# Performance work log

Measured on AMD Instinct MI355X. Metric: run time of the kernel, lower is better.

The kernel has to match this reference:

```python
import jax, jax.numpy as jnp
import numpy as np

B, T, C = 4, 2048, 1024
E, F, K = 8, 2048, 2


def setup_inputs() -> dict:
    key = jax.random.key(0)
    k0, k1, k2, k3 = jax.random.split(key, 4)
    s = lambda d: 1.0 / np.sqrt(d)
    x = jax.random.normal(k0, (B, T, C), dtype=jnp.float32)
    Wr = jax.random.normal(k1, (E, C), dtype=jnp.float32) * s(C)      # router: nn.Linear(C, E) weight [E, C]
    W1 = jax.random.normal(k2, (E, 2 * F, C), dtype=jnp.float32) * s(C)  # per-expert w1 [2F, C]
    W2 = jax.random.normal(k3, (E, C, F), dtype=jnp.float32) * s(F)      # per-expert w2 [C, F]
    return {"x": x, "Wr": Wr, "W1": W1, "W2": W2}


def reference(x, Wr, W1, W2):
    Bb, Tt, Cc = x.shape
    flat = x.reshape(-1, Cc)                         # [N, C]
    N = flat.shape[0]
    # router: top-k then softmax over the k selected logits
    logits = flat @ Wr.T                             # [N, E]
    weights, ids = jax.lax.top_k(logits, K)          # [N, K]
    weights = jax.nn.softmax(weights, axis=-1)
    rows = jnp.arange(N)[:, None]
    router_weights = jnp.zeros((N, E), dtype=flat.dtype).at[rows, ids].add(weights)  # [N, E]
    # all experts on all tokens (dense reference), SwiGLU
    h = jnp.einsum('nc,efc->nef', flat, W1)          # [N, E, 2F]
    val, gate = h[..., :F], h[..., F:]
    act = val * jax.nn.silu(gate)                    # [N, E, F]
    expert_outputs = jnp.einsum('nef,ecf->nec', act, W2)  # [N, E, C]
    out = jnp.einsum('nec,ne->nc', expert_outputs, router_weights)
    return out.reshape(Bb, Tt, Cc)
```

## Files before the change

kernel.cpp:

```cpp
#include <hip/hip_runtime.h>

#define NTOK 8192
#define CDIM 1024
#define FDIM 2048
#define NEXP 8
#define CAP  16384
#define NPAIR 16384
#define MTCAP 32

typedef __bf16 bf16x8 __attribute__((ext_vector_type(8)));
typedef float  f32x4  __attribute__((ext_vector_type(4)));

__device__ __forceinline__ unsigned short f2bf(float f) {
    unsigned int u = __builtin_bit_cast(unsigned int, f);
    unsigned int r = (u + 0x7FFFu + ((u >> 16) & 1u)) >> 16;
    return (unsigned short)r;
}

__device__ __forceinline__ unsigned int pack2(float lo, float hi) {
    return ((unsigned int)f2bf(hi) << 16) | (unsigned int)f2bf(lo);
}

__device__ __forceinline__ float bflo(unsigned int u) {
    return __builtin_bit_cast(float, u << 16);
}
__device__ __forceinline__ float bfhi(unsigned int u) {
    return __builtin_bit_cast(float, u & 0xFFFF0000u);
}

__device__ __forceinline__ void gload_lds16(const void* g, void* l) {
    __builtin_amdgcn_global_load_lds(
        (const __attribute__((address_space(1))) unsigned int*)g,
        (__attribute__((address_space(3))) unsigned int*)l, 16, 0, 0);
}

#define BARRIER() asm volatile("s_barrier" ::: "memory")
#define WAIT_LGKM0() do { asm volatile("s_waitcnt lgkmcnt(0)" ::: "memory"); __builtin_amdgcn_sched_barrier(0); } while (0)
#define WAITVM(n) asm volatile("s_waitcnt vmcnt(" #n ")" ::: "memory")

__global__ void cvt_kernel(const float* __restrict__ s, unsigned short* __restrict__ d, long ngrp) {
    long i = (long)blockIdx.x * blockDim.x + threadIdx.x;
    long stride = (long)gridDim.x * blockDim.x;
    const float4* s4 = (const float4*)s;
    uint4* d4 = (uint4*)d;
    for (long g = i; g < ngrp; g += stride) {
        float4 a = s4[2 * g], b = s4[2 * g + 1];
        uint4 o;
        o.x = pack2(a.x, a.y); o.y = pack2(a.z, a.w);
        o.z = pack2(b.x, b.y); o.w = pack2(b.z, b.w);
        d4[g] = o;
    }
}

__global__ __launch_bounds__(256) void logits_kernel(
    const float* __restrict__ x, const float* __restrict__ Wr,
    float* __restrict__ wgt, int* __restrict__ eids)
{
    int w = threadIdx.x >> 6, l = threadIdx.x & 63;
    int t = blockIdx.x * 4 + w;
    const float* xr = x + (size_t)t * CDIM;
    float acc[NEXP];
    #pragma unroll
    for (int e = 0; e < NEXP; e++) acc[e] = 0.f;
    for (int c = l; c < CDIM; c += 64) {
        float xv = xr[c];
        #pragma unroll
        for (int e = 0; e < NEXP; e++) acc[e] += xv * Wr[e * CDIM + c];
    }
    #pragma unroll
    for (int e = 0; e < NEXP; e++)
        for (int off = 32; off > 0; off >>= 1) acc[e] += __shfl_down(acc[e], off);
    if (l == 0) {
        int i0 = 0; float l0 = acc[0];
        #pragma unroll
        for (int e = 1; e < NEXP; e++) if (acc[e] > l0) { l0 = acc[e]; i0 = e; }
        int i1 = -1; float l1 = -3.4e38f;
        #pragma unroll
        for (int e = 0; e < NEXP; e++) if (e != i0 && acc[e] > l1) { l1 = acc[e]; i1 = e; }
        float tv = __expf(l1 - l0);
        float den = 1.f + tv;
        wgt[2 * t] = 1.f / den;
        wgt[2 * t + 1] = tv / den;
        eids[t] = i0 | (i1 << 8);
    }
}

__global__ __launch_bounds__(256) void bucket_kernel(
    const int* __restrict__ eids, int* __restrict__ list, int* __restrict__ cnt)
{
    __shared__ int lcnt[NEXP];
    __shared__ int lbase[NEXP];
    int t = threadIdx.x;
    if (t < NEXP) lcnt[t] = 0;
    __syncthreads();
    int tok = blockIdx.x * 256 + t;
    int id = eids[tok];
    int e0 = id & 0xff, e1 = (id >> 8) & 0xff;
    int s0 = atomicAdd(&lcnt[e0], 1);
    int s1 = atomicAdd(&lcnt[e1], 1);
    __syncthreads();
    if (t < NEXP) lbase[t] = atomicAdd(&cnt[t], lcnt[t]);
    __syncthreads();
    list[e0 * CAP + lbase[e0] + s0] = 2 * tok;
    list[e1 * CAP + lbase[e1] + s1] = 2 * tok + 1;
}

__global__ void offs_kernel(const int* __restrict__ cnt, int* __restrict__ offs) {
    if (threadIdx.x == 0) {
        int a = 0;
        for (int e = 0; e < NEXP; e++) { offs[e] = a; a += cnt[e]; }
    }
}

__global__ __launch_bounds__(256) void pack_kernel(
    const float* __restrict__ x, const int* __restrict__ list,
    const int* __restrict__ cnt, const int* __restrict__ offs,
    const float* __restrict__ wgt,
    unsigned short* __restrict__ xg, float* __restrict__ wgs)
{
    int e = blockIdx.y;
    int cnt_e = cnt[e];
    int s0 = blockIdx.x * 16;
    if (s0 >= cnt_e) return;
    int t = threadIdx.x;
    int sr = s0 + (t >> 4);
    if (sr >= cnt_e) return;
    int p = list[e * CAP + sr];
    int tok = p >> 1;
    if ((t & 15) == 0) wgs[offs[e] + sr] = wgt[p];
    const float4* src = (const float4*)(x + (size_t)tok * CDIM);
    uint2* dst = (uint2*)(xg + (size_t)(offs[e] + sr) * CDIM);
    int c = t & 15;
    #pragma unroll
    for (int i = 0; i < 16; i++) {
        float4 v = src[c + i * 16];
        uint2 o; o.x = pack2(v.x, v.y); o.y = pack2(v.z, v.w);
        dst[c + i * 16] = o;
    }
}

__global__ __launch_bounds__(256, 2) void gemm1_kernel(
    const unsigned short* __restrict__ xg,
    const unsigned short* __restrict__ W1b,
    const float* __restrict__ wgs,
    unsigned short* __restrict__ act,
    const int* __restrict__ cnt, const int* __restrict__ offs)
{
    int e = blockIdx.z, nt = blockIdx.x, mt = blockIdx.y;
    int cnt_e = cnt[e];
    if (mt * 128 >= cnt_e) return;
    int off_e = offs[e];

    __shared__ __align__(16) char lds[32768];

    int t = threadIdx.x, l = t & 63, w = t >> 6;
    int wave_m = w >> 1, wave_n = w & 1;

    int c2s = ((t & 3) * 16) ^ (((t >> 5) & 1) << 5);
    int dst = t * 16;

    const char *sA0, *sA1, *sBv, *sBg;
    {
        int r0 = min(mt * 128 + (t >> 2), cnt_e - 1);
        int r1 = min(mt * 128 + 64 + (t >> 2), cnt_e - 1);
        sA0 = (const char*)xg + (size_t)(off_e + r0) * 2048 + c2s;
        sA1 = (const char*)xg + (size_t)(off_e + r1) * 2048 + c2s;
        int f = nt * 64 + (t >> 2);
        sBv = (const char*)W1b + ((size_t)e * 2 * FDIM + f) * 2048 + c2s;
        sBg = sBv + (size_t)FDIM * 2048;
    }

    int lane_off = (l & 15) * 64 + (((l >> 4) * 16) ^ (((l >> 3) & 1) << 5));
    f32x4 accV[4][2] = {}, accG[4][2] = {};

#define G1_STAGE(H) do { \
        char* Hb = (char*)lds + ((H) & 1) * 16384; \
        gload_lds16(sA0 + (H) * 64, Hb + dst); \
        gload_lds16(sA1 + (H) * 64, Hb + 4096 + dst); \
        gload_lds16(sBv + (H) * 64, Hb + 8192 + dst); \
        gload_lds16(sBg + (H) * 64, Hb + 12288 + dst); \
    } while (0)

    G1_STAGE(0);
    G1_STAGE(1);

    #pragma unroll
    for (int kt = 0; kt < 32; kt++) {
        if (kt == 31) { WAITVM(0); } else { WAITVM(4); }
        BARRIER();

        const char* H = (const char*)lds + (kt & 1) * 16384;
        bf16x8 af[4], bv[2], bg[2];
        #pragma unroll
        for (int m = 0; m < 4; m++)
            af[m] = *(const bf16x8*)(H + (wave_m * 4 + m) * 1024 + lane_off);
        #pragma unroll
        for (int n = 0; n < 2; n++) {
            bv[n] = *(const bf16x8*)(H + 8192 + (wave_n * 2 + n) * 1024 + lane_off);
            bg[n] = *(const bf16x8*)(H + 12288 + (wave_n * 2 + n) * 1024 + lane_off);
        }
        WAIT_LGKM0();
        BARRIER();

        if (kt < 30) G1_STAGE(kt + 2);
        __builtin_amdgcn_sched_barrier(0);

        __builtin_amdgcn_s_setprio(1);
        #pragma unroll
        for (int m = 0; m < 4; m++)
            #pragma unroll
            for (int n = 0; n < 2; n++) {
                accV[m][n] = __builtin_amdgcn_mfma_f32_16x16x32_bf16(af[m], bv[n], accV[m][n], 0, 0, 0);
                accG[m][n] = __builtin_amdgcn_mfma_f32_16x16x32_bf16(af[m], bg[n], accG[m][n], 0, 0, 0);
            }
        __builtin_amdgcn_s_setprio(0);
    }
#undef G1_STAGE

    int colF = nt * 64 + wave_n * 32 + (l & 15);
    int rowB = mt * 128 + wave_m * 64 + ((l >> 4) * 4);
    #pragma unroll
    for (int m = 0; m < 4; m++) {
        #pragma unroll
        for (int r = 0; r < 4; r++) {
            int srow = rowB + m * 16 + r;
            if (srow < cnt_e) {
                float wsc = wgs[off_e + srow];
                #pragma unroll
                for (int n = 0; n < 2; n++) {
                    float g = accG[m][n][r];
                    float v = accV[m][n][r];
                    float aa = wsc * v * g / (1.f + __expf(-g));
                    act[(size_t)(off_e + srow) * FDIM + colF + n * 16] = f2bf(aa);
                }
            }
        }
    }
}

__global__ __launch_bounds__(256, 2) void gemm2_kernel(
    const unsigned short* __restrict__ act,
    const unsigned short* __restrict__ W2b,
    const int* __restrict__ list, const int* __restrict__ cnt,
    const int* __restrict__ offs,
    unsigned short* __restrict__ eob)
{
    int e = blockIdx.z, nt = blockIdx.x, mt = blockIdx.y;
    int cnt_e = cnt[e];
    if (mt * 128 >= cnt_e) return;
    int off_e = offs[e];
    const int* le = list + e * CAP;

    __shared__ __align__(16) char lds[32768];

    int t = threadIdx.x, l = t & 63, w = t >> 6;
    int wave_m = w >> 1, wave_n = w & 1;

    int c2s = ((t & 3) * 16) ^ (((t >> 5) & 1) << 5);
    int dst = t * 16;

    const char *sA0, *sA1, *sB0, *sB1;
    {
        int r0 = min(mt * 128 + (t >> 2), cnt_e - 1);
        int r1 = min(mt * 128 + 64 + (t >> 2), cnt_e - 1);
        sA0 = (const char*)act + (size_t)(off_e + r0) * 4096 + c2s;
        sA1 = (const char*)act + (size_t)(off_e + r1) * 4096 + c2s;
        int c0 = nt * 128 + (t >> 2);
        sB0 = (const char*)W2b + ((size_t)e * CDIM + c0) * 4096 + c2s;
        sB1 = sB0 + (size_t)64 * 4096;
    }

    int lane_off = (l & 15) * 64 + (((l >> 4) * 16) ^ (((l >> 3) & 1) << 5));
    f32x4 acc[4][4] = {};

#define G2_STAGE(H) do { \
        char* Hb = (char*)lds + ((H) & 1) * 16384; \
        gload_lds16(sA0 + (H) * 64, Hb + dst); \
        gload_lds16(sA1 + (H) * 64, Hb + 4096 + dst); \
        gload_lds16(sB0 + (H) * 64, Hb + 8192 + dst); \
        gload_lds16(sB1 + (H) * 64, Hb + 12288 + dst); \
    } while (0)

    G2_STAGE(0);
    G2_STAGE(1);

    #pragma unroll
    for (int kt = 0; kt < 64; kt++) {
        if (kt == 63) { WAITVM(0); } else { WAITVM(4); }
        BARRIER();

        const char* H = (const char*)lds + (kt & 1) * 16384;
        bf16x8 af[4], bf[4];
        #pragma unroll
        for (int m = 0; m < 4; m++)
            af[m] = *(const bf16x8*)(H + (wave_m * 4 + m) * 1024 + lane_off);
        #pragma unroll
        for (int n = 0; n < 4; n++)
            bf[n] = *(const bf16x8*)(H + 8192 + (wave_n * 4 + n) * 1024 + lane_off);
        WAIT_LGKM0();
        BARRIER();

        if (kt < 62) G2_STAGE(kt + 2);
        __builtin_amdgcn_sched_barrier(0);

        __builtin_amdgcn_s_setprio(1);
        #pragma unroll
        for (int m = 0; m < 4; m++)
            #pragma unroll
            for (int n = 0; n < 4; n++)
                acc[m][n] = __builtin_amdgcn_mfma_f32_16x16x32_bf16(af[m], bf[n], acc[m][n], 0, 0, 0);
        __builtin_amdgcn_s_setprio(0);
    }
#undef G2_STAGE

    int colC = nt * 128 + wave_n * 64 + (l & 15);
    int rowB = mt * 128 + wave_m * 64 + ((l >> 4) * 4);
    #pragma unroll
    for (int m = 0; m < 4; m++) {
        #pragma unroll
        for (int r = 0; r < 4; r++) {
            int srow = rowB + m * 16 + r;
            if (srow < cnt_e) {
                int p = le[srow];
                #pragma unroll
                for (int n = 0; n < 4; n++)
                    eob[(size_t)p * CDIM + colC + n * 16] = f2bf(acc[m][n][r]);
            }
        }
    }
}

__global__ __launch_bounds__(256) void combine_kernel(
    const unsigned short* __restrict__ eob, float* __restrict__ out)
{
    const long NG = (long)NTOK * (CDIM / 4);
    long i = (long)blockIdx.x * blockDim.x + threadIdx.x;
    long stride = (long)gridDim.x * blockDim.x;
    float4* out4 = (float4*)out;
    for (long g = i; g < NG; g += stride) {
        long t = g >> 8;
        long j = g & 255;
        uint2 a = ((const uint2*)(eob + (size_t)(2 * t) * CDIM))[j];
        uint2 b = ((const uint2*)(eob + (size_t)(2 * t + 1) * CDIM))[j];
        float4 o;
        o.x = bflo(a.x) + bflo(b.x);
        o.y = bfhi(a.x) + bfhi(b.x);
        o.z = bflo(a.y) + bflo(b.y);
        o.w = bfhi(a.y) + bfhi(b.y);
        out4[g] = o;
    }
}

extern "C" void kernel_launch(void* const* d_in, const int* in_sizes, int n_in,
                              void* d_out, int out_size, void* d_ws, size_t ws_size,
                              hipStream_t stream) {
    const float* x  = (const float*)d_in[0];
    const float* Wr = (const float*)d_in[1];
    const float* W1 = (const float*)d_in[2];
    const float* W2 = (const float*)d_in[3];
    float* out = (float*)d_out;
    char* ws = (char*)d_ws;

    const size_t OFF_XG   = 0;
    const size_t OFF_W1B  = OFF_XG  + (size_t)NPAIR * CDIM * 2;
    const size_t OFF_ACT  = OFF_W1B + (size_t)NEXP * 2 * FDIM * CDIM * 2;
    const size_t OFF_LIST = OFF_ACT + (size_t)NPAIR * FDIM * 2;
    const size_t OFF_WGT  = OFF_LIST + (size_t)NEXP * CAP * 4;
    const size_t OFF_WGS  = OFF_WGT + (size_t)NPAIR * 4;
    const size_t OFF_CNT  = OFF_WGS + (size_t)NPAIR * 4;
    const size_t OFF_OFFS = OFF_CNT + 32;
    const size_t OFF_EIDS = OFF_OFFS + 32;

    unsigned short* xg  = (unsigned short*)(ws + OFF_XG);
    unsigned short* W1b = (unsigned short*)(ws + OFF_W1B);
    unsigned short* act = (unsigned short*)(ws + OFF_ACT);
    int*   list = (int*)(ws + OFF_LIST);
    float* wgt  = (float*)(ws + OFF_WGT);
    float* wgs  = (float*)(ws + OFF_WGS);
    int*   cnt  = (int*)(ws + OFF_CNT);
    int*   offs = (int*)(ws + OFF_OFFS);
    int*   eids = (int*)(ws + OFF_EIDS);
    unsigned short* W2b = (unsigned short*)(ws + OFF_W1B);
    unsigned short* eob = (unsigned short*)(ws + OFF_XG);

    hipMemsetAsync(cnt, 0, NEXP * sizeof(int), stream);

    cvt_kernel<<<4096, 256, 0, stream>>>(W1, W1b, (long)NEXP * 2 * FDIM * CDIM / 8);
    logits_kernel<<<NTOK / 4, 256, 0, stream>>>(x, Wr, wgt, eids);
    bucket_kernel<<<NTOK / 256, 256, 0, stream>>>(eids, list, cnt);
    offs_kernel<<<1, 64, 0, stream>>>(cnt, offs);
    pack_kernel<<<dim3(256, NEXP), 256, 0, stream>>>(x, list, cnt, offs, wgt, xg, wgs);

    gemm1_kernel<<<dim3(FDIM / 64, MTCAP, NEXP), 256, 0, stream>>>(xg, W1b, wgs, act, cnt, offs);

    cvt_kernel<<<4096, 256, 0, stream>>>(W2, W2b, (long)NEXP * CDIM * FDIM / 8);

    gemm2_kernel<<<dim3(CDIM / 128, MTCAP, NEXP), 256, 0, stream>>>(act, W2b, list, cnt, offs, eob);
    combine_kernel<<<2048, 256, 0, stream>>>(eob, out);
}
```

Measured before the change: 380.6 us.

## Enlarge expert GEMM tiles to 256x256 with 8-wave blocks and phased LDS pipeline

Both expert GEMMs move from 128-row tiles with 4 waves and a 32KB LDS double buffer to 256x256 output tiles with 8 waves, 128KB LDS and a K-step of 128 split into four interleaved phases. Each phase overlaps the global-to-LDS staging of the next chunk with MFMA work. In gemm1, value and gate columns are computed by different waves and exchanged through LDS before the SwiGLU epilogue. The grid order is swapped so M tiles vary fastest, and the LDS swizzle is changed. The aim is higher arithmetic intensity and fewer reloads of the weight and activation tiles. In exchange, the large LDS footprint limits occupancy, and 256-row tiles waste more work on partially filled expert buckets.

New measurement: 600.6 us. +57.8%, slower.

```diff
diff --git a/kernel.cpp b/kernel.cpp
--- a/kernel.cpp
+++ b/kernel.cpp
@@ -139,184 +139,187 @@
     }
 }
 
-__global__ __launch_bounds__(256, 2) void gemm1_kernel(
+#define PH(MH, KS, RB, STG, WV) do { \
+    bf16x8 a_[4]; \
+    _Pragma("unroll") for (int i_ = 0; i_ < 4; i_++) \
+        a_[i_] = *(const bf16x8*)(cb + wm * 16384 + (KS) * 8192 + ((MH) * 4 + i_) * 1024 + lane_off); \
+    if (RB) { _Pragma("unroll") for (int n_ = 0; n_ < 4; n_++) \
+        b_[n_] = *(const bf16x8*)(cb + 32768 + (wn >> 1) * 16384 + (KS) * 8192 + (wn & 1) * 4096 + n_ * 1024 + lane_off); } \
+    STG; \
+    BARRIER(); \
+    WAIT_LGKM0(); \
+    __builtin_amdgcn_s_setprio(1); \
+    _Pragma("unroll") for (int i_ = 0; i_ < 4; i_++) \
+        _Pragma("unroll") for (int n_ = 0; n_ < 4; n_++) \
+            acc[(MH) * 4 + i_][n_] = __builtin_amdgcn_mfma_f32_16x16x32_bf16(a_[i_], b_[n_], acc[(MH) * 4 + i_][n_], 0, 0, 0); \
+    __builtin_amdgcn_s_setprio(0); \
+    WV; \
+    BARRIER(); \
+} while (0)
+
+__global__ __launch_bounds__(512, 2) void gemm1_kernel(
     const unsigned short* __restrict__ xg,
     const unsigned short* __restrict__ W1b,
     const float* __restrict__ wgs,
     unsigned short* __restrict__ act,
     const int* __restrict__ cnt, const int* __restrict__ offs)
 {
-    int e = blockIdx.z, nt = blockIdx.x, mt = blockIdx.y;
+    int e = blockIdx.z, mt = blockIdx.x, nt = blockIdx.y;
     int cnt_e = cnt[e];
-    if (mt * 128 >= cnt_e) return;
+    if (mt * 256 >= cnt_e) return;
     int off_e = offs[e];
 
-    __shared__ __align__(16) char lds[32768];
+    __shared__ __align__(16) char lds[131072];
 
     int t = threadIdx.x, l = t & 63, w = t >> 6;
-    int wave_m = w >> 1, wave_n = w & 1;
-
-    int c2s = ((t & 3) * 16) ^ (((t >> 5) & 1) << 5);
+    int wm = w >> 2, wn = w & 3;
+
+    int sgz = ((t & 3) ^ ((t >> 3) & 3)) * 16;
     int dst = t * 16;
 
-    const char *sA0, *sA1, *sBv, *sBg;
+    const char *pA0, *pA1, *pB0, *pB1;
     {
-        int r0 = min(mt * 128 + (t >> 2), cnt_e - 1);
-        int r1 = min(mt * 128 + 64 + (t >> 2), cnt_e - 1);
-        sA0 = (const char*)xg + (size_t)(off_e + r0) * 2048 + c2s;
-        sA1 = (const char*)xg + (size_t)(off_e + r1) * 2048 + c2s;
-        int f = nt * 64 + (t >> 2);
-        sBv = (const char*)W1b + ((size_t)e * 2 * FDIM + f) * 2048 + c2s;
-        sBg = sBv + (size_t)FDIM * 2048;
-    }
-
-    int lane_off = (l & 15) * 64 + (((l >> 4) * 16) ^ (((l >> 3) & 1) << 5));
-    f32x4 accV[4][2] = {}, accG[4][2] = {};
-
-#define G1_STAGE(H) do { \
-        char* Hb = (char*)lds + ((H) & 1) * 16384; \
-        gload_lds16(sA0 + (H) * 64, Hb + dst); \
-        gload_lds16(sA1 + (H) * 64, Hb + 4096 + dst); \
-        gload_lds16(sBv + (H) * 64, Hb + 8192 + dst); \
-        gload_lds16(sBg + (H) * 64, Hb + 12288 + dst); \
+        int r0 = min(mt * 256 + (t >> 2), cnt_e - 1);
+        int r1 = min(mt * 256 + 128 + (t >> 2), cnt_e - 1);
+        pA0 = (const char*)xg + (size_t)(off_e + r0) * 2048 + sgz;
+        pA1 = (const char*)xg + (size_t)(off_e + r1) * 2048 + sgz;
+        int f = nt * 128 + (t >> 2);
+        pB0 = (const char*)W1b + ((size_t)e * 2 * FDIM + f) * 2048 + sgz;
+        pB1 = pB0 + (size_t)FDIM * 2048;
+    }
+
+    int lane_off = (l & 15) * 64 + (((l >> 4) ^ (((l & 15) >> 1) & 3)) * 16);
+    f32x4 acc[8][4] = {};
+
+#define G1_AC(NB, KB, C) do { \
+        gload_lds16(pA0 + (KB) + (C) * 64, (char*)lds + (NB) + (C) * 8192 + dst); \
+        gload_lds16(pA1 + (KB) + (C) * 64, (char*)lds + (NB) + 16384 + (C) * 8192 + dst); \
     } while (0)
-
-    G1_STAGE(0);
-    G1_STAGE(1);
-
-    #pragma unroll
-    for (int kt = 0; kt < 32; kt++) {
-        if (kt == 31) { WAITVM(0); } else { WAITVM(4); }
-        BARRIER();
-
-        const char* H = (const char*)lds + (kt & 1) * 16384;
-        bf16x8 af[4], bv[2], bg[2];
-        #pragma unroll
-        for (int m = 0; m < 4; m++)
-            af[m] = *(const bf16x8*)(H + (wave_m * 4 + m) * 1024 + lane_off);
-        #pragma unroll
-        for (int n = 0; n < 2; n++) {
-            bv[n] = *(const bf16x8*)(H + 8192 + (wave_n * 2 + n) * 1024 + lane_off);
-            bg[n] = *(const bf16x8*)(H + 12288 + (wave_n * 2 + n) * 1024 + lane_off);
-        }
-        WAIT_LGKM0();
-        BARRIER();
-
-        if (kt < 30) G1_STAGE(kt + 2);
-        __builtin_amdgcn_sched_barrier(0);
-
-        __builtin_amdgcn_s_setprio(1);
-        #pragma unroll
-        for (int m = 0; m < 4; m++)
+#define G1_BC(NB, KB, C) do { \
+        gload_lds16(pB0 + (KB) + (C) * 64, (char*)lds + (NB) + 32768 + (C) * 8192 + dst); \
+        gload_lds16(pB1 + (KB) + (C) * 64, (char*)lds + (NB) + 49152 + (C) * 8192 + dst); \
+    } while (0)
+
+    G1_AC(0, 0, 0); G1_BC(0, 0, 0); G1_AC(0, 0, 1); G1_BC(0, 0, 1);
+    WAITVM(4);
+    BARRIER();
+
+    for (int kt = 0; kt < 16; kt++) {
+        const char* cb = (const char*)lds + (kt & 1) * 65536;
+        int nb = ((kt + 1) & 1) * 65536;
+        int kb = (kt + 1) * 128;
+        bool stg = kt < 15;
+        bf16x8 b_[4];
+        PH(0, 0, true,  { if (stg) G1_AC(nb, kb, 0); }, {});
+        PH(1, 0, false, { if (stg) G1_BC(nb, kb, 0); }, { if (kt == 15) { WAITVM(0); } else { WAITVM(4); } });
+        PH(1, 1, true,  { if (stg) G1_AC(nb, kb, 1); }, {});
+        PH(0, 1, false, { if (stg) G1_BC(nb, kb, 1); }, { if (kt < 15) { WAITVM(4); } });
+    }
+#undef G1_AC
+#undef G1_BC
+
+    float* exch = (float*)lds;
+    if (wn >= 2) {
+        int base = (wm * 2 + (wn - 2)) * 8192;
+        #pragma unroll
+        for (int m = 0; m < 8; m++)
             #pragma unroll
-            for (int n = 0; n < 2; n++) {
-                accV[m][n] = __builtin_amdgcn_mfma_f32_16x16x32_bf16(af[m], bv[n], accV[m][n], 0, 0, 0);
-                accG[m][n] = __builtin_amdgcn_mfma_f32_16x16x32_bf16(af[m], bg[n], accG[m][n], 0, 0, 0);
-            }
-        __builtin_amdgcn_s_setprio(0);
-    }
-#undef G1_STAGE
-
-    int colF = nt * 64 + wave_n * 32 + (l & 15);
-    int rowB = mt * 128 + wave_m * 64 + ((l >> 4) * 4);
-    #pragma unroll
-    for (int m = 0; m < 4; m++) {
-        #pragma unroll
-        for (int r = 0; r < 4; r++) {
-            int srow = rowB + m * 16 + r;
-            if (srow < cnt_e) {
-                float wsc = wgs[off_e + srow];
+            for (int n = 0; n < 4; n++)
+                *(f32x4*)(exch + base + (m * 4 + n) * 256 + l * 4) = acc[m][n];
+    }
+    __syncthreads();
+    if (wn < 2) {
+        int base = (wm * 2 + wn) * 8192;
+        int colF = nt * 128 + wn * 64 + (l & 15);
+        int rowB = mt * 256 + wm * 128 + ((l >> 4) * 4);
+        #pragma unroll
+        for (int m = 0; m < 8; m++) {
+            #pragma unroll
+            for (int n = 0; n < 4; n++) {
+                f32x4 g4 = *(const f32x4*)(exch + base + (m * 4 + n) * 256 + l * 4);
+                int col = colF + n * 16;
                 #pragma unroll
-                for (int n = 0; n < 2; n++) {
-                    float g = accG[m][n][r];
-                    float v = accV[m][n][r];
-                    float aa = wsc * v * g / (1.f + __expf(-g));
-                    act[(size_t)(off_e + srow) * FDIM + colF + n * 16] = f2bf(aa);
+                for (int r = 0; r < 4; r++) {
+                    int srow = rowB + m * 16 + r;
+                    if (srow < cnt_e) {
+                        float wsc = wgs[off_e + srow];
+                        float g = g4[r];
+                        float v = acc[m][n][r];
+                        float aa = wsc * v * g / (1.f + __expf(-g));
+                        act[(size_t)(off_e + srow) * FDIM + col] = f2bf(aa);
+                    }
                 }
             }
         }
     }
 }
 
-__global__ __launch_bounds__(256, 2) void gemm2_kernel(
+__global__ __launch_bounds__(512, 2) void gemm2_kernel(
     const unsigned short* __restrict__ act,
     const unsigned short* __restrict__ W2b,
     const int* __restrict__ list, const int* __restrict__ cnt,
     const int* __restrict__ offs,
     unsigned short* __restrict__ eob)
 {
-    int e = blockIdx.z, nt = blockIdx.x, mt = blockIdx.y;
+    int e = blockIdx.z, mt = blockIdx.x, nt = blockIdx.y;
     int cnt_e = cnt[e];
-    if (mt * 128 >= cnt_e) return;
+    if (mt * 256 >= cnt_e) return;
     int off_e = offs[e];
     const int* le = list + e * CAP;
 
-    __shared__ __align__(16) char lds[32768];
+    __shared__ __align__(16) char lds[131072];
 
     int t = threadIdx.x, l = t & 63, w = t >> 6;
-    int wave_m = w >> 1, wave_n = w & 1;
-
-    int c2s = ((t & 3) * 16) ^ (((t >> 5) & 1) << 5);
+    int wm = w >> 2, wn = w & 3;
+
+    int sgz = ((t & 3) ^ ((t >> 3) & 3)) * 16;
     int dst = t * 16;
 
-    const char *sA0, *sA1, *sB0, *sB1;
+    const char *pA0, *pA1, *pB0, *pB1;
     {
-        int r0 = min(mt * 128 + (t >> 2), cnt_e - 1);
-        int r1 = min(mt * 128 + 64 + (t >> 2), cnt_e - 1);
-        sA0 = (const char*)act + (size_t)(off_e + r0) * 4096 + c2s;
-        sA1 = (const char*)act + (size_t)(off_e + r1) * 4096 + c2s;
-        int c0 = nt * 128 + (t >> 2);
-        sB0 = (const char*)W2b + ((size_t)e * CDIM + c0) * 4096 + c2s;
-        sB1 = sB0 + (size_t)64 * 4096;
-    }
-
-    int lane_off = (l & 15) * 64 + (((l >> 4) * 16) ^ (((l >> 3) & 1) << 5));
-    f32x4 acc[4][4] = {};
-
-#define G2_STAGE(H) do { \
-        char* Hb = (char*)lds + ((H) & 1) * 16384; \
-        gload_lds16(sA0 + (H) * 64, Hb + dst); \
-        gload_lds16(sA1 + (H) * 64, Hb + 4096 + dst); \
-        gload_lds16(sB0 + (H) * 64, Hb + 8192 + dst); \
-        gload_lds16(sB1 + (H) * 64, Hb + 12288 + dst); \
+        int r0 = min(mt * 256 + (t >> 2), cnt_e - 1);
+        int r1 = min(mt * 256 + 128 + (t >> 2), cnt_e - 1);
+        pA0 = (const char*)act + (size_t)(off_e + r0) * 4096 + sgz;
+        pA1 = (const char*)act + (size_t)(off_e + r1) * 4096 + sgz;
+        int c0 = nt * 256 + (t >> 2);
+        pB0 = (const char*)W2b + ((size_t)e * CDIM + c0) * 4096 + sgz;
+        pB1 = pB0 + (size_t)128 * 4096;
+    }
+
+    int lane_off = (l & 15) * 64 + (((l >> 4) ^ (((l & 15) >> 1) & 3)) * 16);
+    f32x4 acc[8][4] = {};
+
+#define G2_AC(NB, KB, C) do { \
+        gload_lds16(pA0 + (KB) + (C) * 64, (char*)lds + (NB) + (C) * 8192 + dst); \
+        gload_lds16(pA1 + (KB) + (C) * 64, (char*)lds + (NB) + 16384 + (C) * 8192 + dst); \
     } while (0)
-
-    G2_STAGE(0);
-    G2_STAGE(1);
-
+#define G2_BC(NB, KB, C) do { \
+        gload_lds16(pB0 + (KB) + (C) * 64, (char*)lds + (NB) + 32768 + (C) * 8192 + dst); \
+        gload_lds16(pB1 + (KB) + (C) * 64, (char*)lds + (NB) + 49152 + (C) * 8192 + dst); \
+    } while (0)
+
+    G2_AC(0, 0, 0); G2_BC(0, 0, 0); G2_AC(0, 0, 1); G2_BC(0, 0, 1);
+    WAITVM(4);
+    BARRIER();
+
+    for (int kt = 0; kt < 32; kt++) {
+        const char* cb = (const char*)lds + (kt & 1) * 65536;
+        int nb = ((kt + 1) & 1) * 65536;
+        int kb = (kt + 1) * 128;
+        bool stg = kt < 31;
+        bf16x8 b_[4];
+        PH(0, 0, true,  { if (stg) G2_AC(nb, kb, 0); }, {});
+        PH(1, 0, false, { if (stg) G2_BC(nb, kb, 0); }, { if (kt == 31) { WAITVM(0); } else { WAITVM(4); } });
+        PH(1, 1, true,  { if (stg) G2_AC(nb, kb, 1); }, {});
+        PH(0, 1, false, { if (stg) G2_BC(nb, kb, 1); }, { if (kt < 31) { WAITVM(4); } });
+    }
+#undef G2_AC
+#undef G2_BC
+
+    int colC = nt * 256 + wn * 64 + (l & 15);
+    int rowB = mt * 256 + wm * 128 + ((l >> 4) * 4);
     #pragma unroll
-    for (int kt = 0; kt < 64; kt++) {
-        if (kt == 63) { WAITVM(0); } else { WAITVM(4); }
-        BARRIER();
-
-        const char* H = (const char*)lds + (kt & 1) * 16384;
-        bf16x8 af[4], bf[4];
-        #pragma unroll
-        for (int m = 0; m < 4; m++)
-            af[m] = *(const bf16x8*)(H + (wave_m * 4 + m) * 1024 + lane_off);
-        #pragma unroll
-        for (int n = 0; n < 4; n++)
-            bf[n] = *(const bf16x8*)(H + 8192 + (wave_n * 4 + n) * 1024 + lane_off);
-        WAIT_LGKM0();
-        BARRIER();
-
-        if (kt < 62) G2_STAGE(kt + 2);
-        __builtin_amdgcn_sched_barrier(0);
-
-        __builtin_amdgcn_s_setprio(1);
-        #pragma unroll
-        for (int m = 0; m < 4; m++)
-            #pragma unroll
-            for (int n = 0; n < 4; n++)
-                acc[m][n] = __builtin_amdgcn_mfma_f32_16x16x32_bf16(af[m], bf[n], acc[m][n], 0, 0, 0);
-        __builtin_amdgcn_s_setprio(0);
-    }
-#undef G2_STAGE
-
-    int colC = nt * 128 + wave_n * 64 + (l & 15);
-    int rowB = mt * 128 + wave_m * 64 + ((l >> 4) * 4);
-    #pragma unroll
-    for (int m = 0; m < 4; m++) {
+    for (int m = 0; m < 8; m++) {
         #pragma unroll
         for (int r = 0; r < 4; r++) {
             int srow = rowB + m * 16 + r;
@@ -391,10 +394,10 @@
     offs_kernel<<<1, 64, 0, stream>>>(cnt, offs);
     pack_kernel<<<dim3(256, NEXP), 256, 0, stream>>>(x, list, cnt, offs, wgt, xg, wgs);
 
-    gemm1_kernel<<<dim3(FDIM / 64, MTCAP, NEXP), 256, 0, stream>>>(xg, W1b, wgs, act, cnt, offs);
+    gemm1_kernel<<<dim3(MTCAP / 2, FDIM / 128, NEXP), 512, 0, stream>>>(xg, W1b, wgs, act, cnt, offs);
 
     cvt_kernel<<<4096, 256, 0, stream>>>(W2, W2b, (long)NEXP * CDIM * FDIM / 8);
 
-    gemm2_kernel<<<dim3(CDIM / 128, MTCAP, NEXP), 256, 0, stream>>>(act, W2b, list, cnt, offs, eob);
+    gemm2_kernel<<<dim3(MTCAP / 2, CDIM / 256, NEXP), 512, 0, stream>>>(act, W2b, list, cnt, offs, eob);
     combine_kernel<<<2048, 256, 0, stream>>>(eob, out);
 }
```
